# Kernel optimization log

Measured on AMD Instinct MI355X. Metric: run time of the kernel, lower is better.

Reference implementation:

```python
import jax, jax.numpy as jnp
import numpy as np

B, T, D = 16, 4096, 1024
HID = 4 * D // 3  # 1365, per SelectorMLP(hidden=4*d//3)
RHO, TAU, LN_EPS = 0.2, 1.0, 1e-5


def setup_inputs() -> dict:
    key = jax.random.key(0)
    ks = jax.random.split(key, 6)
    embeddings = jax.random.normal(ks[0], (B, T, D), dtype=jnp.float32)
    attn = (jax.random.uniform(ks[1], (B, T)) < 0.9).astype(jnp.float32)
    ln_w = jnp.ones((D,), jnp.float32)
    ln_b = jnp.zeros((D,), jnp.float32)
    fc1_w = jax.random.normal(ks[2], (HID, D), jnp.float32) * (1.0 / np.sqrt(D))
    fc1_b = jnp.zeros((HID,), jnp.float32)
    fc2_w = jax.random.normal(ks[3], (1, HID), jnp.float32) * (1.0 / np.sqrt(HID))
    fc2_b = jnp.zeros((1,), jnp.float32)
    return {"embeddings": embeddings, "attn": attn, "ln_w": ln_w, "ln_b": ln_b,
            "fc1_w": fc1_w, "fc1_b": fc1_b, "fc2_w": fc2_w, "fc2_b": fc2_b}


def _hard_topk(z, K):
    # z: [B,T], K: [B,1] float integer budgets -> exact top-K 0/1 mask per row
    b, t = z.shape
    order = jnp.argsort(-z, axis=1)                       # descending sort indices
    mask = (jnp.arange(t)[None, :] < K).astype(z.dtype)   # [B,T] first-K ranks
    h = jnp.zeros_like(z).at[jnp.arange(b)[:, None], order].set(mask)
    return h


def reference(embeddings, attn, ln_w, ln_b, fc1_w, fc1_b, fc2_w, fc2_b):
    emb = embeddings * attn[:, :, None]                    # [B,T,D]
    # SelectorMLP (dropout = identity in eval)
    mu = jnp.mean(emb, axis=-1, keepdims=True)
    var = jnp.mean(jnp.square(emb - mu), axis=-1, keepdims=True)
    x = (emb - mu) / jnp.sqrt(var + LN_EPS) * ln_w + ln_b
    x = jax.nn.gelu(jnp.einsum('btd,hd->bth', x, fc1_w) + fc1_b, approximate=False)
    scores = jnp.einsum('bth,oh->bto', x, fc2_w)[..., 0] + fc2_b[0]  # [B,T]
    scores = jnp.where(attn == 0, -1e9, scores)
    p = jax.nn.softmax(scores / TAU, axis=1)
    entropy = -jnp.sum(p * jnp.log(p + 1e-12), axis=1)     # [B]
    T_eff = jnp.clip(jnp.sum(attn, axis=1), 1, None)
    norm_entropy = jnp.mean(entropy / jnp.log(T_eff))
    T_eff2 = jnp.sum(attn, axis=1, keepdims=True)          # [B,1]
    K = jnp.clip(jnp.round(RHO * T_eff2), 1, None)
    z = K * p
    h = _hard_topk(z, K)
    g = h + (z - jax.lax.stop_gradient(z))                 # straight-through
    return g, z, norm_entropy
```

## Files before the change

### kernel.cpp

```cpp
#include <hip/hip_runtime.h>
#include <math.h>

#define B_ 16
#define T_ 4096
#define D_ 1024
#define HID_ 1365
#define NPAD 1408
#define NGRP 88
#define N_TOK (B_*T_)
#define RHO_ 0.2f
#define LN_EPS_ 1e-5f
#define SC 1024.0f
#define INV_SC2 (1.0f/(1024.0f*1024.0f))

#define NHT 11
#define WCHUNKS (NGRP*32*4*16)
#define NG16 4096
#define ACHUNKS ((size_t)NG16*32*64)

typedef _Float16 f16x8 __attribute__((ext_vector_type(8)));
typedef float f32x4 __attribute__((ext_vector_type(4)));

__device__ __forceinline__ void gl16(const void* g, void* l) {
  __builtin_amdgcn_global_load_lds(
      (const __attribute__((address_space(1))) unsigned int*)g,
      (__attribute__((address_space(3))) unsigned int*)l, 16, 0, 0);
}

__global__ __launch_bounds__(256) void wsplit_kernel(
    const float* __restrict__ fc1w, f16x8* __restrict__ whi, f16x8* __restrict__ wlo)
{
  int c = blockIdx.x * 256 + threadIdx.x;
  if (c >= WCHUNKS) return;
  int ln = c & 15, q = (c >> 4) & 3, ks = (c >> 6) & 31, g = c >> 11;
  int n = g * 16 + ln;
  int k = ks * 32 + q * 8;
  f16x8 hi, lo;
#pragma unroll
  for (int j = 0; j < 8; ++j) {
    float v = (n < HID_) ? fc1w[(size_t)n * D_ + k + j] * SC : 0.f;
    _Float16 h = (_Float16)v;
    hi[j] = h;
    lo[j] = (_Float16)(v - (float)h);
  }
  whi[c] = hi;
  wlo[c] = lo;
}

#define FSTR 1028
__global__ __launch_bounds__(256, 2) void lnasplit_kernel(
    const float* __restrict__ emb, const float* __restrict__ attn,
    const float* __restrict__ lnw, const float* __restrict__ lnb,
    f16x8* __restrict__ ahi, f16x8* __restrict__ alo)
{
  __shared__ float tile[16 * FSTR];
  __shared__ float smu[16], srs[16];
  int tid = threadIdx.x;
  int g = blockIdx.x;
  int wave = tid >> 6, lane = tid & 63;
#pragma unroll
  for (int it = 0; it < 16; ++it) {
    int idx = tid + it * 256;
    int row = idx >> 8, c4 = idx & 255;
    float a = attn[g * 16 + row];
    float4 v = *reinterpret_cast<const float4*>(
        emb + (size_t)(g * 16 + row) * D_ + c4 * 4);
    v.x *= a; v.y *= a; v.z *= a; v.w *= a;
    *reinterpret_cast<float4*>(&tile[row * FSTR + c4 * 4]) = v;
  }
  __syncthreads();
#pragma unroll
  for (int r4 = 0; r4 < 4; ++r4) {
    int row = wave * 4 + r4;
    float s = 0.f, sq = 0.f;
#pragma unroll
    for (int q = 0; q < 4; ++q) {
      float4 v = *reinterpret_cast<const float4*>(&tile[row * FSTR + lane * 4 + q * 256]);
      s  += v.x + v.y + v.z + v.w;
      sq += v.x * v.x + v.y * v.y + v.z * v.z + v.w * v.w;
    }
#pragma unroll
    for (int off = 32; off > 0; off >>= 1) {
      s  += __shfl_down(s, off, 64);
      sq += __shfl_down(sq, off, 64);
    }
    if (lane == 0) {
      float m = s * (1.f / D_);
      float var = sq * (1.f / D_) - m * m;
      if (var < 0.f) var = 0.f;
      smu[row] = m;
      srs[row] = 1.f / sqrtf(var + LN_EPS_);
    }
  }
  __syncthreads();
#pragma unroll
  for (int it = 0; it < 8; ++it) {
    int idx = tid + it * 256;
    int ksl = idx >> 6, l = idx & 63;
    int ln = l & 15, q = l >> 4;
    float rs = srs[ln];
    float nmr = -smu[ln] * rs;
    int colbase = ksl * 32 + q * 8;
    float4 e0 = *reinterpret_cast<const float4*>(&tile[ln * FSTR + colbase]);
    float4 e1 = *reinterpret_cast<const float4*>(&tile[ln * FSTR + colbase + 4]);
    float ev[8] = {e0.x, e0.y, e0.z, e0.w, e1.x, e1.y, e1.z, e1.w};
    f16x8 hi, lo;
#pragma unroll
    for (int j = 0; j < 8; ++j) {
      int kg = colbase + j;
      float wv = lnw[kg], bv = lnb[kg];
      float y = fmaf(ev[j] * rs, wv, fmaf(nmr, wv, bv)) * SC;
      _Float16 h = (_Float16)y;
      hi[j] = h;
      lo[j] = (_Float16)(y - (float)h);
    }
    size_t c = (size_t)(g * 32 + ksl) * 64 + l;
    ahi[c] = hi;
    alo[c] = lo;
  }
}

__global__ __launch_bounds__(256, 2) void mfma_score_v5(
    const f16x8* __restrict__ ahi, const f16x8* __restrict__ alo,
    const f16x8* __restrict__ whi, const f16x8* __restrict__ wlo,
    const float* __restrict__ fc1b, const float* __restrict__ fc2w,
    float* __restrict__ partial)
{
  __shared__ f16x8 sbuf[2][2048];
  __shared__ float red[2][128];
  int tid = threadIdx.x, lane = tid & 63;
  int w = tid >> 6, wrow = w & 1, wcol = w >> 1;
  int flat = blockIdx.x;
  int xcd = flat & 7, j = flat >> 3;
  int tb = xcd * 64 + j / NHT;
  int ht = j % NHT;
  int g0 = tb * 8;
  int hb0 = ht * 8;
  int ln16 = lane & 15, quad = lane >> 4;

  const f16x8* src = (w == 0) ? ahi : (w == 1) ? alo : (w == 2) ? whi : wlo;
  size_t grpbase = (w < 2) ? (size_t)g0 : (size_t)hb0;
  const f16x8* sp = src + grpbase * 32 * 64 + lane;

  auto STAGE = [&](int buf, int ks) {
#pragma unroll
    for (int i = 0; i < 8; ++i)
      gl16(sp + (size_t)(i * 32 + ks) * 64, &sbuf[buf][w * 512 + i * 64]);
  };

  STAGE(0, 0);

  f32x4 acc[4][4];
#pragma unroll
  for (int i = 0; i < 4; ++i)
#pragma unroll
    for (int j2 = 0; j2 < 4; ++j2) acc[i][j2] = (f32x4)0.f;

  __syncthreads();

#pragma unroll 2
  for (int ks = 0; ks < 32; ++ks) {
    int cur = ks & 1;
    if (ks < 31) STAGE(cur ^ 1, ks + 1);
    f16x8 ah[4], al[4], bh[4], bl[4];
#pragma unroll
    for (int mi = 0; mi < 4; ++mi) {
      ah[mi] = sbuf[cur][(wrow * 4 + mi) * 64 + lane];
      al[mi] = sbuf[cur][512 + (wrow * 4 + mi) * 64 + lane];
    }
#pragma unroll
    for (int nj = 0; nj < 4; ++nj) {
      bh[nj] = sbuf[cur][1024 + (wcol * 4 + nj) * 64 + lane];
      bl[nj] = sbuf[cur][1536 + (wcol * 4 + nj) * 64 + lane];
    }
#pragma unroll
    for (int mi = 0; mi < 4; ++mi)
#pragma unroll
      for (int nj = 0; nj < 4; ++nj) {
        acc[mi][nj] = __builtin_amdgcn_mfma_f32_16x16x32_f16(ah[mi], bh[nj], acc[mi][nj], 0, 0, 0);
        acc[mi][nj] = __builtin_amdgcn_mfma_f32_16x16x32_f16(al[mi], bh[nj], acc[mi][nj], 0, 0, 0);
        acc[mi][nj] = __builtin_amdgcn_mfma_f32_16x16x32_f16(ah[mi], bl[nj], acc[mi][nj], 0, 0, 0);
      }
    __syncthreads();
  }

  int gb0 = hb0 + wcol * 4;
  float s[4][4];
#pragma unroll
  for (int mi = 0; mi < 4; ++mi)
#pragma unroll
    for (int r = 0; r < 4; ++r) s[mi][r] = 0.f;
#pragma unroll
  for (int nj = 0; nj < 4; ++nj) {
    int h = (gb0 + nj) * 16 + ln16;
    float b1 = 0.f, w2 = 0.f;
    if (h < HID_) { b1 = fc1b[h]; w2 = fc2w[h]; }
#pragma unroll
    for (int mi = 0; mi < 4; ++mi)
#pragma unroll
      for (int r = 0; r < 4; ++r) {
        float v = acc[mi][nj][r] * INV_SC2 + b1;
        float gel = 0.5f * v * (1.f + erff(v * 0.70710678118654752440f));
        s[mi][r] = fmaf(gel, w2, s[mi][r]);
      }
  }
#pragma unroll
  for (int mi = 0; mi < 4; ++mi)
#pragma unroll
    for (int r = 0; r < 4; ++r) {
      float v = s[mi][r];
      v += __shfl_xor(v, 1, 64);
      v += __shfl_xor(v, 2, 64);
      v += __shfl_xor(v, 4, 64);
      v += __shfl_xor(v, 8, 64);
      s[mi][r] = v;
    }
  if (ln16 == 0) {
#pragma unroll
    for (int mi = 0; mi < 4; ++mi)
#pragma unroll
      for (int r = 0; r < 4; ++r)
        red[wcol][wrow * 64 + mi * 16 + quad * 4 + r] = s[mi][r];
  }
  __syncthreads();
  if (tid < 128)
    partial[(size_t)ht * N_TOK + tb * 128 + tid] = red[0][tid] + red[1][tid];
}

__global__ __launch_bounds__(1024) void softmax_kernel(
    const float* __restrict__ partial, const float* __restrict__ fc2b,
    const float* __restrict__ attn,
    float* __restrict__ out_z, float* __restrict__ rowent, float* __restrict__ rowK)
{
  __shared__ float buf[1024];
  int b = blockIdx.x, tid = threadIdx.x;
  const float* arow = attn + b * T_;
  float sv[4], av[4];
  float f2b = fc2b[0];
#pragma unroll
  for (int q = 0; q < 4; ++q) {
    int t = tid + q * 1024;
    av[q] = arow[t];
    float sc = f2b;
#pragma unroll
    for (int p = 0; p < NHT; ++p) sc += partial[(size_t)p * N_TOK + b * T_ + t];
    sv[q] = (av[q] == 0.f) ? -1e9f : sc;
  }
  float m = fmaxf(fmaxf(sv[0], sv[1]), fmaxf(sv[2], sv[3]));
  buf[tid] = m; __syncthreads();
  for (int s = 512; s > 0; s >>= 1) { if (tid < s) buf[tid] = fmaxf(buf[tid], buf[tid + s]); __syncthreads(); }
  m = buf[0]; __syncthreads();
  float e[4]; float es = 0.f, as = 0.f;
#pragma unroll
  for (int q = 0; q < 4; ++q) { e[q] = expf(sv[q] - m); es += e[q]; as += av[q]; }
  buf[tid] = es; __syncthreads();
  for (int s = 512; s > 0; s >>= 1) { if (tid < s) buf[tid] += buf[tid + s]; __syncthreads(); }
  es = buf[0]; __syncthreads();
  buf[tid] = as; __syncthreads();
  for (int s = 512; s > 0; s >>= 1) { if (tid < s) buf[tid] += buf[tid + s]; __syncthreads(); }
  as = buf[0]; __syncthreads();
  float K = fmaxf(1.f, rintf(RHO_ * as));
  float inv = 1.f / es;
  float ent = 0.f;
#pragma unroll
  for (int q = 0; q < 4; ++q) {
    float p = e[q] * inv;
    out_z[b * T_ + tid + q * 1024] = K * p;
    ent -= p * logf(p + 1e-12f);
  }
  buf[tid] = ent; __syncthreads();
  for (int s = 512; s > 0; s >>= 1) { if (tid < s) buf[tid] += buf[tid + s]; __syncthreads(); }
  if (tid == 0) {
    rowent[b] = buf[0] / logf(fmaxf(as, 1.f));
    rowK[b] = K;
  }
}

__global__ __launch_bounds__(1024) void topk_kernel(
    const float* __restrict__ zall, float* __restrict__ g,
    const float* __restrict__ rowent, const float* __restrict__ rowK,
    float* __restrict__ out_scalar)
{
  __shared__ float sm[T_];
  __shared__ int s_first, s_last;
  int b = blockIdx.x, tid = threadIdx.x;
  const float* zrow = zall + b * T_;
  for (int t = tid; t < T_; t += 1024) sm[t] = zrow[t];
  __syncthreads();
  for (int k = 2; k <= T_; k <<= 1) {
    for (int j = k >> 1; j > 0; j >>= 1) {
      for (int t = tid; t < T_; t += 1024) {
        int ixj = t ^ j;
        if (ixj > t) {
          float a = sm[t], c = sm[ixj];
          bool desc = ((t & k) == 0);
          if (desc ? (a < c) : (a > c)) { sm[t] = c; sm[ixj] = a; }
        }
      }
      __syncthreads();
    }
  }
  int K = (int)rowK[b];
  float thr = sm[K - 1];
  if (tid == 0) { s_first = T_; s_last = -1; }
  __syncthreads();
  for (int t = tid; t < T_; t += 1024) {
    if (sm[t] == thr) { atomicMin(&s_first, t); atomicMax(&s_last, t); }
  }
  __syncthreads();
  int cgt = s_first;
  int eqTotal = s_last - s_first + 1;
  int need = K - cgt;
  float* grow = g + b * T_;
  bool allEq = (eqTotal == need);
  for (int t = tid; t < T_; t += 1024) {
    float zv = zrow[t];
    if (zv > thr) grow[t] = 1.f;
    else if (zv < thr) grow[t] = 0.f;
    else if (allEq) grow[t] = 1.f;
  }
  __syncthreads();
  if (!allEq && tid == 0) {
    int cnt = 0;
    for (int t = 0; t < T_; ++t) {
      float zv = zrow[t];
      if (zv == thr) { grow[t] = (cnt < need) ? 1.f : 0.f; ++cnt; }
    }
  }
  if (b == 0 && tid == 0) {
    float s = 0.f;
    for (int i = 0; i < B_; ++i) s += rowent[i];
    out_scalar[0] = s * (1.f / B_);
  }
}

extern "C" void kernel_launch(void* const* d_in, const int* in_sizes, int n_in,
                              void* d_out, int out_size, void* d_ws, size_t ws_size,
                              hipStream_t stream)
{
  const float* emb  = (const float*)d_in[0];
  const float* attn = (const float*)d_in[1];
  const float* lnw  = (const float*)d_in[2];
  const float* lnb  = (const float*)d_in[3];
  const float* fc1w = (const float*)d_in[4];
  const float* fc1b = (const float*)d_in[5];
  const float* fc2w = (const float*)d_in[6];
  const float* fc2b = (const float*)d_in[7];

  float* out = (float*)d_out;
  float* g  = out;
  float* z  = out + N_TOK;
  float* ns = out + 2 * N_TOK;

  float* mu      = (float*)d_ws;
  float* rstd    = mu + N_TOK;
  float* partial = rstd + N_TOK;
  float* rowent  = partial + (size_t)NHT * N_TOK;
  float* rowK    = rowent + 16;
  f16x8* whi     = (f16x8*)(rowK + 16);
  f16x8* wlo     = whi + WCHUNKS;
  f16x8* ahi     = wlo + WCHUNKS;
  f16x8* alo     = ahi + ACHUNKS;

  wsplit_kernel<<<(WCHUNKS + 255) / 256, 256, 0, stream>>>(fc1w, whi, wlo);
  lnasplit_kernel<<<NG16, 256, 0, stream>>>(emb, attn, lnw, lnb, ahi, alo);
  mfma_score_v5<<<8 * 64 * NHT, 256, 0, stream>>>(ahi, alo, whi, wlo, fc1b, fc2w, partial);
  softmax_kernel<<<B_, 1024, 0, stream>>>(partial, fc2b, attn, z, rowent, rowK);
  topk_kernel<<<B_, 1024, 0, stream>>>(z, g, rowent, rowK, ns);
}
```

Measured before the change: 1.080 ms.

## Enlarge MFMA token tile, interleave LDS loads with MFMA phases, radix-select top-k

The score GEMM kernel now uses 512-thread blocks with 8 waves covering 256 tokens per block instead of 128, which doubles reuse of each staged weight tile. The K-loop is split into three MFMA phases (hi*hi, lo*hi, hi*lo), each with its own LDS fetch and raw barriers, and raises wave priority around the MFMA bursts to overlap loads with math. Separately, the bitonic sort in top-k is replaced by a 4-pass 8-bit radix select on the float bit patterns to find the K-th threshold. This relies on z being non-negative so the unsigned bit order matches float order, and adds extra barriers and LDS pressure in the GEMM.

```diff
diff --git a/kernel.cpp b/kernel.cpp
--- a/kernel.cpp
+++ b/kernel.cpp
@@ -120,35 +120,43 @@
   }
 }
 
-__global__ __launch_bounds__(256, 2) void mfma_score_v5(
+__global__ __launch_bounds__(512, 2) void mfma_score_v7(
     const f16x8* __restrict__ ahi, const f16x8* __restrict__ alo,
     const f16x8* __restrict__ whi, const f16x8* __restrict__ wlo,
     const float* __restrict__ fc1b, const float* __restrict__ fc2w,
     float* __restrict__ partial)
 {
-  __shared__ f16x8 sbuf[2][2048];
-  __shared__ float red[2][128];
+  __shared__ f16x8 sbuf[2][3072];
+  __shared__ float red[2][256];
   int tid = threadIdx.x, lane = tid & 63;
-  int w = tid >> 6, wrow = w & 1, wcol = w >> 1;
+  int w = tid >> 6, wrow = w & 3, wcol = w >> 2;
   int flat = blockIdx.x;
   int xcd = flat & 7, j = flat >> 3;
-  int tb = xcd * 64 + j / NHT;
+  int tb = xcd * 32 + j / NHT;
   int ht = j % NHT;
-  int g0 = tb * 8;
+  int g0 = tb * 16;
   int hb0 = ht * 8;
   int ln16 = lane & 15, quad = lane >> 4;
 
-  const f16x8* src = (w == 0) ? ahi : (w == 1) ? alo : (w == 2) ? whi : wlo;
-  size_t grpbase = (w < 2) ? (size_t)g0 : (size_t)hb0;
-  const f16x8* sp = src + grpbase * 32 * 64 + lane;
-
-  auto STAGE = [&](int buf, int ks) {
-#pragma unroll
-    for (int i = 0; i < 8; ++i)
-      gl16(sp + (size_t)(i * 32 + ks) * 64, &sbuf[buf][w * 512 + i * 64]);
-  };
-
-  STAGE(0, 0);
+  int u0 = w * 6;
+  const f16x8* sp[6];
+#pragma unroll
+  for (int i = 0; i < 6; ++i) {
+    int u = u0 + i;
+    const f16x8* base;
+    int grp;
+    if (u < 16)      { base = ahi; grp = g0 + u; }
+    else if (u < 32) { base = alo; grp = g0 + (u - 16); }
+    else if (u < 40) { base = whi; grp = hb0 + (u - 32); }
+    else             { base = wlo; grp = hb0 + (u - 40); }
+    sp[i] = base + (size_t)grp * 2048 + lane;
+  }
+
+#define PBAR() do { __builtin_amdgcn_sched_barrier(0); \
+                    __builtin_amdgcn_s_barrier();      \
+                    __builtin_amdgcn_sched_barrier(0); } while (0)
+#define LG0()  do { asm volatile("s_waitcnt lgkmcnt(0)" ::: "memory"); \
+                    __builtin_amdgcn_sched_barrier(0); } while (0)
 
   f32x4 acc[4][4];
 #pragma unroll
@@ -156,33 +164,75 @@
 #pragma unroll
     for (int j2 = 0; j2 < 4; ++j2) acc[i][j2] = (f32x4)0.f;
 
-  __syncthreads();
-
-#pragma unroll 2
+#pragma unroll
+  for (int i = 0; i < 6; ++i)
+    gl16(sp[i], &sbuf[0][(u0 + i) * 64]);
+  __builtin_amdgcn_sched_barrier(0);
+  asm volatile("s_waitcnt vmcnt(0)" ::: "memory");
+  __builtin_amdgcn_s_barrier();
+  __builtin_amdgcn_sched_barrier(0);
+
+#pragma unroll 1
   for (int ks = 0; ks < 32; ++ks) {
     int cur = ks & 1;
-    if (ks < 31) STAGE(cur ^ 1, ks + 1);
-    f16x8 ah[4], al[4], bh[4], bl[4];
-#pragma unroll
-    for (int mi = 0; mi < 4; ++mi) {
-      ah[mi] = sbuf[cur][(wrow * 4 + mi) * 64 + lane];
-      al[mi] = sbuf[cur][512 + (wrow * 4 + mi) * 64 + lane];
-    }
-#pragma unroll
-    for (int nj = 0; nj < 4; ++nj) {
-      bh[nj] = sbuf[cur][1024 + (wcol * 4 + nj) * 64 + lane];
-      bl[nj] = sbuf[cur][1536 + (wcol * 4 + nj) * 64 + lane];
-    }
+    const f16x8* sb = &sbuf[cur][0];
+    f16x8* nb = &sbuf[cur ^ 1][0];
+
+    f16x8 ah[4], bh[4];
+#pragma unroll
+    for (int mi = 0; mi < 4; ++mi) ah[mi] = sb[(wrow * 4 + mi) * 64 + lane];
+#pragma unroll
+    for (int nj = 0; nj < 4; ++nj) bh[nj] = sb[2048 + (wcol * 4 + nj) * 64 + lane];
+    if (ks < 31) {
+#pragma unroll
+      for (int i = 0; i < 6; ++i)
+        gl16(sp[i] + (size_t)(ks + 1) * 64, &nb[(u0 + i) * 64]);
+    }
+    PBAR();
+    LG0();
+    __builtin_amdgcn_s_setprio(1);
 #pragma unroll
     for (int mi = 0; mi < 4; ++mi)
 #pragma unroll
-      for (int nj = 0; nj < 4; ++nj) {
+      for (int nj = 0; nj < 4; ++nj)
         acc[mi][nj] = __builtin_amdgcn_mfma_f32_16x16x32_f16(ah[mi], bh[nj], acc[mi][nj], 0, 0, 0);
+    __builtin_amdgcn_s_setprio(0);
+    PBAR();
+
+    f16x8 al[4];
+#pragma unroll
+    for (int mi = 0; mi < 4; ++mi) al[mi] = sb[1024 + (wrow * 4 + mi) * 64 + lane];
+    PBAR();
+    LG0();
+    __builtin_amdgcn_s_setprio(1);
+#pragma unroll
+    for (int mi = 0; mi < 4; ++mi)
+#pragma unroll
+      for (int nj = 0; nj < 4; ++nj)
         acc[mi][nj] = __builtin_amdgcn_mfma_f32_16x16x32_f16(al[mi], bh[nj], acc[mi][nj], 0, 0, 0);
+    __builtin_amdgcn_s_setprio(0);
+    PBAR();
+
+    f16x8 bl[4];
+#pragma unroll
+    for (int nj = 0; nj < 4; ++nj) bl[nj] = sb[2560 + (wcol * 4 + nj) * 64 + lane];
+    PBAR();
+    LG0();
+    __builtin_amdgcn_s_setprio(1);
+#pragma unroll
+    for (int mi = 0; mi < 4; ++mi)
+#pragma unroll
+      for (int nj = 0; nj < 4; ++nj)
         acc[mi][nj] = __builtin_amdgcn_mfma_f32_16x16x32_f16(ah[mi], bl[nj], acc[mi][nj], 0, 0, 0);
-      }
-    __syncthreads();
-  }
+    __builtin_amdgcn_s_setprio(0);
+    __builtin_amdgcn_sched_barrier(0);
+    asm volatile("s_waitcnt vmcnt(0)" ::: "memory");
+    __builtin_amdgcn_s_barrier();
+    __builtin_amdgcn_sched_barrier(0);
+  }
+
+#undef PBAR
+#undef LG0
 
   int gb0 = hb0 + wcol * 4;
   float s[4][4];
@@ -223,8 +273,8 @@
         red[wcol][wrow * 64 + mi * 16 + quad * 4 + r] = s[mi][r];
   }
   __syncthreads();
-  if (tid < 128)
-    partial[(size_t)ht * N_TOK + tb * 128 + tid] = red[0][tid] + red[1][tid];
+  if (tid < 256)
+    partial[(size_t)ht * N_TOK + tb * 256 + tid] = red[0][tid] + red[1][tid];
 }
 
 __global__ __launch_bounds__(1024) void softmax_kernel(
@@ -281,50 +331,71 @@
     const float* __restrict__ rowent, const float* __restrict__ rowK,
     float* __restrict__ out_scalar)
 {
-  __shared__ float sm[T_];
-  __shared__ int s_first, s_last;
+  __shared__ unsigned hist[256];
+  __shared__ unsigned s_prefix, s_kk;
+  __shared__ int s_cgt, s_ceq;
   int b = blockIdx.x, tid = threadIdx.x;
   const float* zrow = zall + b * T_;
-  for (int t = tid; t < T_; t += 1024) sm[t] = zrow[t];
-  __syncthreads();
-  for (int k = 2; k <= T_; k <<= 1) {
-    for (int j = k >> 1; j > 0; j >>= 1) {
-      for (int t = tid; t < T_; t += 1024) {
-        int ixj = t ^ j;
-        if (ixj > t) {
-          float a = sm[t], c = sm[ixj];
-          bool desc = ((t & k) == 0);
-          if (desc ? (a < c) : (a > c)) { sm[t] = c; sm[ixj] = a; }
-        }
+  unsigned zb[4];
+#pragma unroll
+  for (int q = 0; q < 4; ++q) zb[q] = __float_as_uint(zrow[tid + q * 1024]);
+  int K = (int)rowK[b];
+
+  unsigned prefix = 0;
+  unsigned kk = (unsigned)K;
+#pragma unroll
+  for (int pass = 0; pass < 4; ++pass) {
+    int sh = 24 - pass * 8;
+    unsigned pmask = pass ? (0xFFFFFFFFu << (sh + 8)) : 0u;
+    if (tid < 256) hist[tid] = 0;
+    __syncthreads();
+#pragma unroll
+    for (int q = 0; q < 4; ++q) {
+      unsigned v = zb[q];
+      if ((v & pmask) == (prefix & pmask)) atomicAdd(&hist[(v >> sh) & 255], 1u);
+    }
+    __syncthreads();
+    if (tid == 0) {
+      unsigned acc = 0;
+      int bsel = 0;
+      for (int i = 255; i >= 0; --i) {
+        unsigned c = hist[i];
+        if (acc + c >= kk) { bsel = i; s_kk = kk - acc; break; }
+        acc += c;
       }
-      __syncthreads();
-    }
-  }
-  int K = (int)rowK[b];
-  float thr = sm[K - 1];
-  if (tid == 0) { s_first = T_; s_last = -1; }
-  __syncthreads();
-  for (int t = tid; t < T_; t += 1024) {
-    if (sm[t] == thr) { atomicMin(&s_first, t); atomicMax(&s_last, t); }
-  }
-  __syncthreads();
-  int cgt = s_first;
-  int eqTotal = s_last - s_first + 1;
-  int need = K - cgt;
+      s_prefix = prefix | ((unsigned)bsel << sh);
+    }
+    __syncthreads();
+    prefix = s_prefix; kk = s_kk;
+    __syncthreads();
+  }
+  if (tid == 0) { s_cgt = 0; s_ceq = 0; }
+  __syncthreads();
+  int cg = 0, ce = 0;
+#pragma unroll
+  for (int q = 0; q < 4; ++q) {
+    if (zb[q] > prefix) ++cg;
+    else if (zb[q] == prefix) ++ce;
+  }
+  if (cg) atomicAdd(&s_cgt, cg);
+  if (ce) atomicAdd(&s_ceq, ce);
+  __syncthreads();
+  int need = K - s_cgt;
+  bool allEq = (s_ceq == need);
   float* grow = g + b * T_;
-  bool allEq = (eqTotal == need);
-  for (int t = tid; t < T_; t += 1024) {
-    float zv = zrow[t];
-    if (zv > thr) grow[t] = 1.f;
-    else if (zv < thr) grow[t] = 0.f;
+#pragma unroll
+  for (int q = 0; q < 4; ++q) {
+    int t = tid + q * 1024;
+    unsigned v = zb[q];
+    if (v > prefix) grow[t] = 1.f;
+    else if (v < prefix) grow[t] = 0.f;
     else if (allEq) grow[t] = 1.f;
   }
   __syncthreads();
   if (!allEq && tid == 0) {
     int cnt = 0;
     for (int t = 0; t < T_; ++t) {
-      float zv = zrow[t];
-      if (zv == thr) { grow[t] = (cnt < need) ? 1.f : 0.f; ++cnt; }
+      if (__float_as_uint(zrow[t]) == prefix) { grow[t] = (cnt < need) ? 1.f : 0.f; ++cnt; }
     }
   }
   if (b == 0 && tid == 0) {
@@ -364,7 +435,7 @@
 
   wsplit_kernel<<<(WCHUNKS + 255) / 256, 256, 0, stream>>>(fc1w, whi, wlo);
   lnasplit_kernel<<<NG16, 256, 0, stream>>>(emb, attn, lnw, lnb, ahi, alo);
-  mfma_score_v5<<<8 * 64 * NHT, 256, 0, stream>>>(ahi, alo, whi, wlo, fc1b, fc2w, partial);
+  mfma_score_v7<<<8 * 32 * NHT, 512, 0, stream>>>(ahi, alo, whi, wlo, fc1b, fc2w, partial);
   softmax_kernel<<<B_, 1024, 0, stream>>>(partial, fc2b, attn, z, rowent, rowK);
   topk_kernel<<<B_, 1024, 0, stream>>>(z, g, rowent, rowK, ns);
 }
```

New measurement: 1.150 ms. 6.5% more time.
